# Performance work log

Measured on AMD Instinct MI355X. Metric: run time of the kernel, lower is better.

The kernel has to match this reference:

```python
import jax, jax.numpy as jnp
import numpy as np

N_NODES = 50000
N_EDGES = 625000
D = 128


def setup_inputs() -> dict:
    key = jax.random.key(0)
    kx, ks, kr, kw, kb = jax.random.split(key, 5)
    x = jax.random.normal(kx, (N_NODES, D), dtype=jnp.float32)
    senders = jax.random.randint(ks, (N_EDGES,), 0, N_NODES, dtype=jnp.int64)
    receivers = jax.random.randint(kr, (N_EDGES,), 0, N_NODES, dtype=jnp.int64)
    # nn.Linear(2*D, D): weight [D, 2*D], bias [D]
    lim = 1.0 / np.sqrt(2 * D)
    W = jax.random.uniform(kw, (D, 2 * D), minval=-lim, maxval=lim, dtype=jnp.float32)
    b = jax.random.uniform(kb, (D,), minval=-lim, maxval=lim, dtype=jnp.float32)
    return {"x": x, "senders": senders, "receivers": receivers, "n_nodes": N_NODES, "W": W, "b": b}


def reference(x, senders, receivers, n_nodes, W, b):
    # Add self loops (with_self=True)
    self_idx = jnp.arange(n_nodes, dtype=senders.dtype)
    s = jnp.concatenate([senders, self_idx])   # [E + N]
    r = jnp.concatenate([receivers, self_idx]) # [E + N]

    ones = jnp.ones(r.shape[0], dtype=x.dtype)
    # degree_norm=True branch (note: mirrors the original's naming exactly:
    # 'out_degree' counted over receivers, 'in_degree' over senders)
    out_degree = jax.ops.segment_sum(ones, r, num_segments=n_nodes)  # [N]
    in_degree = jax.ops.segment_sum(ones, s, num_segments=n_nodes)   # [N]
    out_degree_norm = jax.lax.rsqrt(jnp.maximum(out_degree, 1.0))
    in_degree_norm = jax.lax.rsqrt(jnp.maximum(in_degree, 1.0))

    # Gather sender embeddings, scale, scatter-add to receivers
    sender_emb = x[s] * out_degree_norm[s][:, None]  # [E+N, D]
    aggregated = jax.ops.segment_sum(sender_emb, r, num_segments=n_nodes)  # [N, D]

    # edge_count over receivers == out_degree (same scatter), clamped
    edge_count = jnp.maximum(out_degree, 1.0)
    aggregated = aggregated / edge_count[:, None]
    aggregated = aggregated * in_degree_norm[:, None]

    combined = jnp.concatenate([x, aggregated], axis=1)  # [N, 2D]
    return combined @ W.T + b
```

## Files before the change

kernel.cpp:

```cpp
#include <hip/hip_runtime.h>

#define DIM 128
#define BM 128
#define BK 32
#define BINSZ 128
#define EPB 2048

typedef __attribute__((ext_vector_type(8))) short short8;
typedef __attribute__((ext_vector_type(4))) float f32x4;

__device__ __forceinline__ unsigned short f2bf(float f) {
    unsigned int b = __float_as_uint(f);
    return (unsigned short)((b + 0x7fffu + ((b >> 16) & 1u)) >> 16);
}
__device__ __forceinline__ float bf_lo(unsigned int u) { return __uint_as_float(u << 16); }
__device__ __forceinline__ float bf_hi(unsigned int u) { return __uint_as_float(u & 0xffff0000u); }
__device__ __forceinline__ unsigned int pack2(float a, float b) {
    return (unsigned int)f2bf(a) | ((unsigned int)f2bf(b) << 16);
}
__device__ __forceinline__ uint2 pack4(float4 v) {
    uint2 r; r.x = pack2(v.x, v.y); r.y = pack2(v.z, v.w); return r;
}

__global__ void convert_kernel(const float4* __restrict__ x4,
                               const float4* __restrict__ W4,
                               uint2* __restrict__ xb4,
                               uint2* __restrict__ Wb4,
                               int nx4, int nw4) {
    int i = blockIdx.x * blockDim.x + threadIdx.x;
    if (i < nx4) xb4[i] = pack4(x4[i]);
    if (i < nw4) Wb4[i] = pack4(W4[i]);
}

__global__ __launch_bounds__(256) void hist_kernel(
        const int* __restrict__ senders, const int* __restrict__ receivers,
        int* __restrict__ Hr, int* __restrict__ Hs, int E, int nbin) {
    __shared__ int hr[512], hs[512];
    int t = threadIdx.x;
    for (int b = t; b < nbin; b += 256) { hr[b] = 0; hs[b] = 0; }
    __syncthreads();
    int base = blockIdx.x * EPB;
    for (int k = 0; k < EPB; k += 256) {
        int e = base + k + t;
        if (e < E) {
            atomicAdd(&hr[receivers[e] >> 7], 1);
            atomicAdd(&hs[senders[e] >> 7], 1);
        }
    }
    __syncthreads();
    size_t ho = (size_t)blockIdx.x * nbin;
    for (int b = t; b < nbin; b += 256) {
        Hr[ho + b] = hr[b];
        Hs[ho + b] = hs[b];
    }
}

__global__ __launch_bounds__(512) void scan_bins_kernel(
        int* __restrict__ Hr, int* __restrict__ Hs,
        int* __restrict__ tot_r, int* __restrict__ tot_s,
        int NAB, int nbin) {
    __shared__ int sr[512], ss[512];
    int b = blockIdx.x, t = threadIdx.x;
    int vr = (t < NAB) ? Hr[(size_t)t * nbin + b] : 0;
    int vs = (t < NAB) ? Hs[(size_t)t * nbin + b] : 0;
    sr[t] = vr; ss[t] = vs;
    __syncthreads();
    for (int off = 1; off < 512; off <<= 1) {
        int ur = (t >= off) ? sr[t - off] : 0;
        int us = (t >= off) ? ss[t - off] : 0;
        __syncthreads();
        sr[t] += ur; ss[t] += us;
        __syncthreads();
    }
    if (t < NAB) {
        Hr[(size_t)t * nbin + b] = sr[t] - vr;
        Hs[(size_t)t * nbin + b] = ss[t] - vs;
    }
    if (t == 511) { tot_r[b] = sr[511]; tot_s[b] = ss[511]; }
}

__global__ __launch_bounds__(512) void scan_base_kernel(
        const int* __restrict__ tot_r, const int* __restrict__ tot_s,
        int* __restrict__ base_r, int* __restrict__ base_s,
        int* __restrict__ row_start, int nbin, int N, int E) {
    __shared__ int sr[512], ss[512];
    int t = threadIdx.x;
    int vr = (t < nbin) ? tot_r[t] : 0;
    int vs = (t < nbin) ? tot_s[t] : 0;
    sr[t] = vr; ss[t] = vs;
    __syncthreads();
    for (int off = 1; off < 512; off <<= 1) {
        int ur = (t >= off) ? sr[t - off] : 0;
        int us = (t >= off) ? ss[t - off] : 0;
        __syncthreads();
        sr[t] += ur; ss[t] += us;
        __syncthreads();
    }
    if (t < nbin) {
        base_r[t] = sr[t] - vr;
        base_s[t] = ss[t] - vs;
    }
    if (t == 0) { base_r[nbin] = E; base_s[nbin] = E; row_start[N] = E; }
}

__global__ __launch_bounds__(256) void scatter_kernel(
        const int* __restrict__ senders, const int* __restrict__ receivers,
        const int* __restrict__ Hr, const int* __restrict__ Hs,
        const int* __restrict__ base_r, const int* __restrict__ base_s,
        unsigned int* __restrict__ bucket_r, int* __restrict__ bucket_s,
        int E, int nbin) {
    __shared__ int br_[512], bs_[512];
    int t = threadIdx.x;
    size_t ho = (size_t)blockIdx.x * nbin;
    for (int b = t; b < nbin; b += 256) {
        br_[b] = base_r[b] + Hr[ho + b];
        bs_[b] = base_s[b] + Hs[ho + b];
    }
    __syncthreads();
    int base = blockIdx.x * EPB;
    for (int k = 0; k < EPB; k += 256) {
        int e = base + k + t;
        if (e < E) {
            int s = senders[e], r = receivers[e];
            int pr = atomicAdd(&br_[r >> 7], 1);
            bucket_r[pr] = ((unsigned int)(r & 127) << 16) | (unsigned int)s;
            int ps = atomicAdd(&bs_[s >> 7], 1);
            bucket_s[ps] = s;
        }
    }
}

__global__ __launch_bounds__(256) void fine_kernel(
        const unsigned int* __restrict__ bucket_r,
        const int* __restrict__ bucket_s,
        const int* __restrict__ base_r,
        const int* __restrict__ base_s,
        const uint2* __restrict__ xb2,
        int* __restrict__ edge_src,
        int* __restrict__ row_start,
        float* __restrict__ fs,
        uint2* __restrict__ xs2,
        int N) {
    __shared__ int fine[BINSZ], fstart[BINSZ], cs[BINSZ];
    __shared__ float scs[BINSZ];
    int b = blockIdx.x, t = threadIdx.x;
    if (t < BINSZ) { fine[t] = 0; cs[t] = 0; }
    __syncthreads();

    int loR = base_r[b], hiR = base_r[b + 1];
    int loS = base_s[b], hiS = base_s[b + 1];
    for (int i = loR + t; i < hiR; i += 256)
        atomicAdd(&fine[bucket_r[i] >> 16], 1);
    for (int i = loS + t; i < hiS; i += 256)
        atomicAdd(&cs[bucket_s[i] & 127], 1);
    __syncthreads();

    if (t < BINSZ) fstart[t] = fine[t];
    __syncthreads();
    for (int off = 1; off < BINSZ; off <<= 1) {
        int u = (t < BINSZ && t >= off) ? fstart[t - off] : 0;
        __syncthreads();
        if (t < BINSZ) fstart[t] += u;
        __syncthreads();
    }
    if (t < BINSZ) {
        int excl = fstart[t] - fine[t];
        int node = b * BINSZ + t;
        float od = (float)(fine[t] + 1);
        float sc = rsqrtf(od);
        scs[t] = sc;
        if (node < N) {
            row_start[node] = loR + excl;
            fs[node] = rsqrtf((float)(cs[t] + 1)) / od;
        }
        fstart[t] = excl;
    }
    __syncthreads();

    for (int i = loR + t; i < hiR; i += 256) {
        unsigned int u = bucket_r[i];
        int pos = atomicAdd(&fstart[u >> 16], 1);
        edge_src[loR + pos] = (int)(u & 0xFFFFu);
    }

    int nrow0 = b * BINSZ;
    for (int idx = t; idx < BINSZ * 32; idx += 256) {
        int row = idx >> 5, c = idx & 31;
        int node = nrow0 + row;
        if (node < N) {
            float sc = scs[row];
            uint2 u = xb2[(size_t)node * 32 + c];
            uint2 o;
            o.x = pack2(bf_lo(u.x) * sc, bf_hi(u.x) * sc);
            o.y = pack2(bf_lo(u.y) * sc, bf_hi(u.y) * sc);
            xs2[(size_t)node * 32 + c] = o;
        }
    }
}

__global__ __launch_bounds__(256) void gather_kernel(
        const unsigned int* __restrict__ xs,
        const int* __restrict__ edge_src,
        const int* __restrict__ row_start,
        const float* __restrict__ fs,
        unsigned int* __restrict__ aggb,
        int N) {
    int lane = threadIdx.x & 63;
    int n = (blockIdx.x * blockDim.x + threadIdx.x) >> 6;
    if (n >= N) return;

    int start = row_start[n];
    int deg   = row_start[n + 1] - start;
    float ax = 0.f, ay = 0.f;

    for (int base = 0; base < deg; base += 64) {
        int cnt = deg - base; if (cnt > 64) cnt = 64;
        int src = 0;
        if (lane < cnt) src = edge_src[start + base + lane];
        int j = 0;
        for (; j + 8 <= cnt; j += 8) {
            int ss[8]; unsigned int uu[8];
#pragma unroll
            for (int q = 0; q < 8; q++) ss[q] = __shfl(src, j + q);
#pragma unroll
            for (int q = 0; q < 8; q++) uu[q] = xs[(size_t)ss[q] * 64 + lane];
#pragma unroll
            for (int q = 0; q < 8; q++) { ax += bf_lo(uu[q]); ay += bf_hi(uu[q]); }
        }
        for (; j < cnt; j++) {
            int s = __shfl(src, j);
            unsigned int u = xs[(size_t)s * 64 + lane];
            ax += bf_lo(u); ay += bf_hi(u);
        }
    }

    float f = fs[n];
    unsigned int u = xs[(size_t)n * 64 + lane];
    ax = (ax + bf_lo(u)) * f;
    ay = (ay + bf_hi(u)) * f;
    aggb[(size_t)n * 64 + lane] = pack2(ax, ay);
}

__global__ __launch_bounds__(512) void gemm_kernel(
        const unsigned short* __restrict__ x_bf,
        const unsigned short* __restrict__ agg_bf,
        const unsigned short* __restrict__ W_bf,
        const float* __restrict__ bias,
        float* __restrict__ out, int N) {
    __shared__ unsigned short As[BM * BK];
    __shared__ unsigned short Bs[DIM * BK];

    int t    = threadIdx.x;
    int lane = t & 63;
    int w    = t >> 6;
    int wr   = w >> 2, wc = w & 3;
    int row0 = blockIdx.x * BM;

    f32x4 acc[4][2];
#pragma unroll
    for (int i = 0; i < 4; i++)
#pragma unroll
        for (int j = 0; j < 2; j++) acc[i][j] = (f32x4){0.f, 0.f, 0.f, 0.f};

    for (int kt = 0; kt < 8; kt++) {
        const unsigned short* src = (kt < 4) ? x_bf : agg_bf;
        int k0 = (kt & 3) * BK;
        {
            int row = t >> 2, ch = t & 3;
            uint4 v = *(const uint4*)&src[(size_t)(row0 + row) * 128 + k0 + ch * 8];
            *(uint4*)&As[row * BK + ch * 8] = v;
        }
        {
            int n = t >> 2, ch = t & 3;
            uint4 v = *(const uint4*)&W_bf[(size_t)n * 256 + kt * BK + ch * 8];
            *(uint4*)&Bs[n * BK + ch * 8] = v;
        }
        __syncthreads();

        short8 a[4], b[2];
#pragma unroll
        for (int i = 0; i < 4; i++)
            a[i] = *(const short8*)&As[(wr * 64 + i * 16 + (lane & 15)) * BK + (lane >> 4) * 8];
#pragma unroll
        for (int j = 0; j < 2; j++)
            b[j] = *(const short8*)&Bs[(wc * 32 + j * 16 + (lane & 15)) * BK + (lane >> 4) * 8];
#pragma unroll
        for (int i = 0; i < 4; i++)
#pragma unroll
            for (int j = 0; j < 2; j++)
                acc[i][j] = __builtin_amdgcn_mfma_f32_16x16x32_bf16(a[i], b[j], acc[i][j], 0, 0, 0);
        __syncthreads();
    }

    int cq = lane >> 4;
    int cl = lane & 15;
#pragma unroll
    for (int j = 0; j < 2; j++) {
        int col = wc * 32 + j * 16 + cl;
        float bb = bias[col];
#pragma unroll
        for (int i = 0; i < 4; i++) {
            int rbase = row0 + wr * 64 + i * 16 + cq * 4;
#pragma unroll
            for (int r = 0; r < 4; r++) {
                int row = rbase + r;
                if (row < N) out[(size_t)row * DIM + col] = acc[i][j][r] + bb;
            }
        }
    }
}

extern "C" void kernel_launch(void* const* d_in, const int* in_sizes, int n_in,
                              void* d_out, int out_size, void* d_ws, size_t ws_size,
                              hipStream_t stream) {
    const float* x         = (const float*)d_in[0];
    const int*   senders   = (const int*)d_in[1];
    const int*   receivers = (const int*)d_in[2];
    const float* W         = (const float*)d_in[4];
    const float* bias      = (const float*)d_in[5];
    float*       out       = (float*)d_out;

    int N    = in_sizes[0] / DIM;
    int E    = in_sizes[1];
    int nbin = (N + BINSZ - 1) / BINSZ;
    int NAB  = (E + EPB - 1) / EPB;
    int NP   = ((N + BM - 1) / BM) * BM;

    char* ws = (char*)d_ws;
    size_t off = 0;
    #define WS_ALLOC(ptrtype, name, bytes) \
        ptrtype name = (ptrtype)(ws + off); off += (((size_t)(bytes)) + 255) & ~(size_t)255;
    WS_ALLOC(int*,            tot_r,     (size_t)nbin * 4)
    WS_ALLOC(int*,            tot_s,     (size_t)nbin * 4)
    WS_ALLOC(int*,            base_r,    (size_t)(nbin + 1) * 4)
    WS_ALLOC(int*,            base_s,    (size_t)(nbin + 1) * 4)
    WS_ALLOC(int*,            row_start, (size_t)(N + 1) * 4)
    WS_ALLOC(float*,          fs,        (size_t)N * 4)
    WS_ALLOC(int*,            edge_src,  (size_t)E * 4)
    WS_ALLOC(unsigned short*, x_bf,      (size_t)NP * DIM * 2)
    WS_ALLOC(unsigned short*, xs_bf,     (size_t)NP * DIM * 2)
    WS_ALLOC(unsigned short*, agg_bf,    (size_t)NP * DIM * 2)
    WS_ALLOC(unsigned short*, W_bf,      (size_t)DIM * 256 * 2)
    #undef WS_ALLOC

    size_t eb = ((size_t)E * 4 + 255) & ~(size_t)255;
    size_t hb = ((size_t)NAB * nbin * 4 + 255) & ~(size_t)255;
    unsigned int* bucket_r = (unsigned int*)agg_bf;
    int*          bucket_s = (int*)((char*)agg_bf + eb);
    int*          Hr       = (int*)((char*)agg_bf + 2 * eb);
    int*          Hs       = (int*)((char*)agg_bf + 2 * eb + hb);

    int nx4 = N * 32;
    int nw4 = DIM * 256 / 4;
    convert_kernel<<<(nx4 + 255) / 256, 256, 0, stream>>>(
        (const float4*)x, (const float4*)W, (uint2*)x_bf, (uint2*)W_bf, nx4, nw4);
    hist_kernel<<<NAB, 256, 0, stream>>>(senders, receivers, Hr, Hs, E, nbin);
    scan_bins_kernel<<<nbin, 512, 0, stream>>>(Hr, Hs, tot_r, tot_s, NAB, nbin);
    scan_base_kernel<<<1, 512, 0, stream>>>(tot_r, tot_s, base_r, base_s,
                                            row_start, nbin, N, E);
    scatter_kernel<<<NAB, 256, 0, stream>>>(senders, receivers, Hr, Hs,
                                            base_r, base_s, bucket_r, bucket_s, E, nbin);
    fine_kernel<<<nbin, 256, 0, stream>>>(bucket_r, bucket_s, base_r, base_s,
                                          (const uint2*)x_bf, edge_src, row_start,
                                          fs, (uint2*)xs_bf, N);
    gather_kernel<<<(N * 64 + 255) / 256, 256, 0, stream>>>(
        (const unsigned int*)xs_bf, edge_src, row_start, fs,
        (unsigned int*)agg_bf, N);
    gemm_kernel<<<(N + BM - 1) / BM, 512, 0, stream>>>(
        x_bf, agg_bf, W_bf, bias, out, N);
}
```

Measured before the change: 176.9 us.

## Fold bf16 conversion into hist/fine kernels and pack four nodes per wave in gather

After: 176.5 us (median of 2 runs). Within noise of the previous version (-0.2%).

```diff
diff --git a/kernel.cpp b/kernel.cpp
--- a/kernel.cpp
+++ b/kernel.cpp
@@ -22,21 +22,16 @@
     uint2 r; r.x = pack2(v.x, v.y); r.y = pack2(v.z, v.w); return r;
 }
 
-__global__ void convert_kernel(const float4* __restrict__ x4,
-                               const float4* __restrict__ W4,
-                               uint2* __restrict__ xb4,
-                               uint2* __restrict__ Wb4,
-                               int nx4, int nw4) {
-    int i = blockIdx.x * blockDim.x + threadIdx.x;
-    if (i < nx4) xb4[i] = pack4(x4[i]);
-    if (i < nw4) Wb4[i] = pack4(W4[i]);
-}
-
 __global__ __launch_bounds__(256) void hist_kernel(
         const int* __restrict__ senders, const int* __restrict__ receivers,
-        int* __restrict__ Hr, int* __restrict__ Hs, int E, int nbin) {
+        const float4* __restrict__ W4, uint2* __restrict__ Wb4,
+        int* __restrict__ Hr, int* __restrict__ Hs, int E, int nbin, int nw4) {
     __shared__ int hr[512], hs[512];
     int t = threadIdx.x;
+
+    int gi = blockIdx.x * 256 + t;
+    if (gi < nw4) Wb4[gi] = pack4(W4[gi]);
+
     for (int b = t; b < nbin; b += 256) { hr[b] = 0; hs[b] = 0; }
     __syncthreads();
     int base = blockIdx.x * EPB;
@@ -135,7 +130,8 @@
         const int* __restrict__ bucket_s,
         const int* __restrict__ base_r,
         const int* __restrict__ base_s,
-        const uint2* __restrict__ xb2,
+        const float4* __restrict__ x4,
+        uint2* __restrict__ xb2,
         int* __restrict__ edge_src,
         int* __restrict__ row_start,
         float* __restrict__ fs,
@@ -188,57 +184,72 @@
         int row = idx >> 5, c = idx & 31;
         int node = nrow0 + row;
         if (node < N) {
+            float4 v = x4[(size_t)node * 32 + c];
             float sc = scs[row];
-            uint2 u = xb2[(size_t)node * 32 + c];
-            uint2 o;
-            o.x = pack2(bf_lo(u.x) * sc, bf_hi(u.x) * sc);
-            o.y = pack2(bf_lo(u.y) * sc, bf_hi(u.y) * sc);
-            xs2[(size_t)node * 32 + c] = o;
+            xb2[(size_t)node * 32 + c] = pack4(v);
+            float4 vs;
+            vs.x = v.x * sc; vs.y = v.y * sc; vs.z = v.z * sc; vs.w = v.w * sc;
+            xs2[(size_t)node * 32 + c] = pack4(vs);
         }
     }
 }
 
 __global__ __launch_bounds__(256) void gather_kernel(
-        const unsigned int* __restrict__ xs,
+        const uint4* __restrict__ xs4,
         const int* __restrict__ edge_src,
         const int* __restrict__ row_start,
         const float* __restrict__ fs,
-        unsigned int* __restrict__ aggb,
+        uint4* __restrict__ aggb4,
         int N) {
     int lane = threadIdx.x & 63;
-    int n = (blockIdx.x * blockDim.x + threadIdx.x) >> 6;
-    if (n >= N) return;
-
-    int start = row_start[n];
-    int deg   = row_start[n + 1] - start;
-    float ax = 0.f, ay = 0.f;
-
-    for (int base = 0; base < deg; base += 64) {
-        int cnt = deg - base; if (cnt > 64) cnt = 64;
-        int src = 0;
-        if (lane < cnt) src = edge_src[start + base + lane];
-        int j = 0;
-        for (; j + 8 <= cnt; j += 8) {
-            int ss[8]; unsigned int uu[8];
-#pragma unroll
-            for (int q = 0; q < 8; q++) ss[q] = __shfl(src, j + q);
-#pragma unroll
-            for (int q = 0; q < 8; q++) uu[q] = xs[(size_t)ss[q] * 64 + lane];
-#pragma unroll
-            for (int q = 0; q < 8; q++) { ax += bf_lo(uu[q]); ay += bf_hi(uu[q]); }
-        }
-        for (; j < cnt; j++) {
-            int s = __shfl(src, j);
-            unsigned int u = xs[(size_t)s * 64 + lane];
-            ax += bf_lo(u); ay += bf_hi(u);
-        }
-    }
-
-    float f = fs[n];
-    unsigned int u = xs[(size_t)n * 64 + lane];
-    ax = (ax + bf_lo(u)) * f;
-    ay = (ay + bf_hi(u)) * f;
-    aggb[(size_t)n * 64 + lane] = pack2(ax, ay);
+    int grp  = lane >> 4;
+    int gl   = lane & 15;
+    int wid  = (blockIdx.x * blockDim.x + threadIdx.x) >> 6;
+    int n    = wid * 4 + grp;
+    bool valid = (n < N);
+
+    int start = 0, deg = 0;
+    if (valid) {
+        start = row_start[n];
+        deg   = row_start[n + 1] - start;
+    }
+    int md = deg;
+    md = max(md, __shfl_xor(md, 16));
+    md = max(md, __shfl_xor(md, 32));
+
+    float a[8];
+#pragma unroll
+    for (int q = 0; q < 8; q++) a[q] = 0.f;
+
+    for (int base = 0; base < md; base += 16) {
+        int e = base + gl;
+        int src = -1;
+        if (e < deg) src = edge_src[start + e];
+#pragma unroll
+        for (int j = 0; j < 16; j++) {
+            int s = __shfl(src, (grp << 4) | j);
+            if (s >= 0) {
+                uint4 u = xs4[(size_t)s * 16 + gl];
+                a[0] += bf_lo(u.x); a[1] += bf_hi(u.x);
+                a[2] += bf_lo(u.y); a[3] += bf_hi(u.y);
+                a[4] += bf_lo(u.z); a[5] += bf_hi(u.z);
+                a[6] += bf_lo(u.w); a[7] += bf_hi(u.w);
+            }
+        }
+    }
+
+    if (valid) {
+        float f = fs[n];
+        uint4 u = xs4[(size_t)n * 16 + gl];
+        a[0] = (a[0] + bf_lo(u.x)) * f; a[1] = (a[1] + bf_hi(u.x)) * f;
+        a[2] = (a[2] + bf_lo(u.y)) * f; a[3] = (a[3] + bf_hi(u.y)) * f;
+        a[4] = (a[4] + bf_lo(u.z)) * f; a[5] = (a[5] + bf_hi(u.z)) * f;
+        a[6] = (a[6] + bf_lo(u.w)) * f; a[7] = (a[7] + bf_hi(u.w)) * f;
+        uint4 o;
+        o.x = pack2(a[0], a[1]); o.y = pack2(a[2], a[3]);
+        o.z = pack2(a[4], a[5]); o.w = pack2(a[6], a[7]);
+        aggb4[(size_t)n * 16 + gl] = o;
+    }
 }
 
 __global__ __launch_bounds__(512) void gemm_kernel(
@@ -350,22 +361,24 @@
     int*          Hr       = (int*)((char*)agg_bf + 2 * eb);
     int*          Hs       = (int*)((char*)agg_bf + 2 * eb + hb);
 
-    int nx4 = N * 32;
     int nw4 = DIM * 256 / 4;
-    convert_kernel<<<(nx4 + 255) / 256, 256, 0, stream>>>(
-        (const float4*)x, (const float4*)W, (uint2*)x_bf, (uint2*)W_bf, nx4, nw4);
-    hist_kernel<<<NAB, 256, 0, stream>>>(senders, receivers, Hr, Hs, E, nbin);
+
+    hist_kernel<<<NAB, 256, 0, stream>>>(senders, receivers,
+                                         (const float4*)W, (uint2*)W_bf,
+                                         Hr, Hs, E, nbin, nw4);
     scan_bins_kernel<<<nbin, 512, 0, stream>>>(Hr, Hs, tot_r, tot_s, NAB, nbin);
     scan_base_kernel<<<1, 512, 0, stream>>>(tot_r, tot_s, base_r, base_s,
                                             row_start, nbin, N, E);
     scatter_kernel<<<NAB, 256, 0, stream>>>(senders, receivers, Hr, Hs,
                                             base_r, base_s, bucket_r, bucket_s, E, nbin);
     fine_kernel<<<nbin, 256, 0, stream>>>(bucket_r, bucket_s, base_r, base_s,
-                                          (const uint2*)x_bf, edge_src, row_start,
-                                          fs, (uint2*)xs_bf, N);
-    gather_kernel<<<(N * 64 + 255) / 256, 256, 0, stream>>>(
-        (const unsigned int*)xs_bf, edge_src, row_start, fs,
-        (unsigned int*)agg_bf, N);
+                                          (const float4*)x, (uint2*)x_bf,
+                                          edge_src, row_start, fs,
+                                          (uint2*)xs_bf, N);
+    int nwave = (N + 3) / 4;
+    gather_kernel<<<(nwave * 64 + 255) / 256, 256, 0, stream>>>(
+        (const uint4*)xs_bf, edge_src, row_start, fs,
+        (uint4*)agg_bf, N);
     gemm_kernel<<<(N + BM - 1) / BM, 512, 0, stream>>>(
         x_bf, agg_bf, W_bf, bias, out, N);
 }
```
